# Optimization experiments

Measured on AMD Instinct MI355X. Metric: run time of the kernel, lower is better.

Reference implementation:

```python
import jax, jax.numpy as jnp
import numpy as np

B, S, H, V, NL = 64, 2048, 512, 50257, 2

def setup_inputs() -> dict:
    key = jax.random.key(0)
    ks = jax.random.split(key, 20)
    s = 0.02
    return {
        "input_ids": jax.random.randint(ks[0], (B,), 0, V),
        "hidden": jax.random.normal(ks[1], (NL, B, H), jnp.float32),
        "block_attn_weights": jax.random.uniform(ks[2], (B, 32), jnp.float32),
        "encoder_outputs": jax.random.normal(ks[3], (B, S, H), jnp.float32),
        "n_blocks": 32,
        "emb": jax.random.normal(ks[4], (V, H), jnp.float32) * s,
        "attn_W": jax.random.normal(ks[5], (H, H), jnp.float32) * s,
        "attn_b": jnp.zeros((H,), jnp.float32),
        "W_ih0": jax.random.normal(ks[6], (3 * H, 2 * H), jnp.float32) * s,
        "W_hh0": jax.random.normal(ks[7], (3 * H, H), jnp.float32) * s,
        "b_ih0": jnp.zeros((3 * H,), jnp.float32),
        "b_hh0": jnp.zeros((3 * H,), jnp.float32),
        "W_ih1": jax.random.normal(ks[8], (3 * H, H), jnp.float32) * s,
        "W_hh1": jax.random.normal(ks[9], (3 * H, H), jnp.float32) * s,
        "b_ih1": jnp.zeros((3 * H,), jnp.float32),
        "b_hh1": jnp.zeros((3 * H,), jnp.float32),
        "out_W": jax.random.normal(ks[10], (V, 2 * H), jnp.float32) * s,
        "out_b": jnp.zeros((V,), jnp.float32),
    }

def _gru_cell(x, h, W_ih, W_hh, b_ih, b_hh):
    gx = x @ W_ih.T + b_ih            # [B, 3H]
    gh = h @ W_hh.T + b_hh            # [B, 3H]
    xr, xz, xn = jnp.split(gx, 3, axis=-1)
    hr, hz, hn = jnp.split(gh, 3, axis=-1)
    r = jax.nn.sigmoid(xr + hr)
    z = jax.nn.sigmoid(xz + hz)
    n = jnp.tanh(xn + r * hn)
    return (1.0 - z) * n + z * h

def reference(input_ids, hidden, block_attn_weights, encoder_outputs, n_blocks,
              emb, attn_W, attn_b, W_ih0, W_hh0, b_ih0, b_hh0,
              W_ih1, W_hh1, b_ih1, b_hh1, out_W, out_b):
    b, s, h = encoder_outputs.shape
    L = s // n_blocks
    eo = encoder_outputs.reshape(b, n_blocks, L, h)          # [B,N,L,H]
    # Luong general score: h_dec . (W e + b), per block
    energy = jnp.einsum('bnlh,gh->bnlg', eo, attn_W) + attn_b  # [B,N,L,H]
    scores = jnp.einsum('bh,bnlh->bnl', hidden[-1], energy)    # [B,N,L]
    attn_w = jax.nn.softmax(scores, axis=-1)                   # [B,N,L]
    block_ctx = jnp.einsum('bnl,bnlh->bnh', attn_w, eo)        # [B,N,H]
    context = jnp.einsum('bn,bnh->bh', block_attn_weights, block_ctx)  # [B,H]
    embedded = emb[input_ids]                                  # [B,H]
    x = jnp.concatenate([embedded, context], axis=-1)          # [B,2H]
    h0 = _gru_cell(x, hidden[0], W_ih0, W_hh0, b_ih0, b_hh0)
    h1 = _gru_cell(h0, hidden[1], W_ih1, W_hh1, b_ih1, b_hh1)
    new_hidden = jnp.stack([h0, h1], axis=0)                   # [NL,B,H]
    out_in = jnp.concatenate([h1, context], axis=-1)           # [B,2H]
    log_probs = jax.nn.log_softmax(out_in @ out_W.T + out_b, axis=-1)  # [B,V]
    return (log_probs, new_hidden, context, attn_w)
```

## Files before the change

kernel.cpp:

```cpp
#include <hip/hip_runtime.h>

#define B_  64
#define S_  2048
#define H_  512
#define V_  50257
#define NB_ 32
#define L_  64
#define H3_ 1536
#define NBLK_OUT 786

typedef float  f32x4  __attribute__((ext_vector_type(4)));
typedef __bf16 bf16x8 __attribute__((ext_vector_type(8)));

struct alignas(16) U4 { unsigned int x, y, z, w; };

__device__ __forceinline__ unsigned int f2bf_bits(float f) {
  unsigned int u = __float_as_uint(f);
  return (u + 0x7fffu + ((u >> 16) & 1u)) >> 16;
}

__device__ __forceinline__ f32x4 ntload4(const float* p) {
  return __builtin_nontemporal_load((const f32x4*)p);
}

__device__ __forceinline__ float wave_sum(float v) {
#pragma unroll
  for (int off = 32; off > 0; off >>= 1) v += __shfl_xor(v, off, 64);
  return v;
}

__global__ __launch_bounds__(128) void k_q(const float* __restrict__ hidden,
                                           const float* __restrict__ attn_W,
                                           float* __restrict__ q) {
  __shared__ float sh[4 * H_];
  int tid = threadIdx.x;
  int h  = blockIdx.x * 128 + tid;
  int b0 = blockIdx.y * 4;
  const float* h1 = hidden + B_ * H_;
  for (int i = tid; i < 4 * H_; i += 128) sh[i] = h1[b0 * H_ + i];
  __syncthreads();
  float acc[4] = {0.f, 0.f, 0.f, 0.f};
  for (int g = 0; g < H_; ++g) {
    float w = attn_W[(size_t)g * H_ + h];
#pragma unroll
    for (int bb = 0; bb < 4; ++bb) acc[bb] += sh[bb * H_ + g] * w;
  }
#pragma unroll
  for (int bb = 0; bb < 4; ++bb) q[(b0 + bb) * H_ + h] = acc[bb];
}

__global__ __launch_bounds__(512) void k_attn(
    const float* __restrict__ eo, const float* __restrict__ hidden,
    const float* __restrict__ attn_b, const float* __restrict__ q,
    float* __restrict__ bc, float* __restrict__ attnw_out) {
  __shared__ float sm[8], ss[8];
  __shared__ float shA[8][H_];
  int tid = threadIdx.x;
  int wv = tid >> 6, lane = tid & 63;
  int idx = blockIdx.x;
  int b = idx >> 5, n = idx & 31;

  f32x4 q0 = *(const f32x4*)(q + (size_t)b * H_ + lane * 4);
  f32x4 q1 = *(const f32x4*)(q + (size_t)b * H_ + 256 + lane * 4);

  const float* hp = hidden + (size_t)B_ * H_ + (size_t)b * H_;
  f32x4 hx = *(const f32x4*)(hp + lane * 4);
  f32x4 hy = *(const f32x4*)(hp + 256 + lane * 4);
  f32x4 ax = *(const f32x4*)(attn_b + lane * 4);
  f32x4 ay = *(const f32x4*)(attn_b + 256 + lane * 4);
  float c0 = hx.x*ax.x + hx.y*ax.y + hx.z*ax.z + hx.w*ax.w
           + hy.x*ay.x + hy.y*ay.y + hy.z*ay.z + hy.w*ay.w;
  c0 = wave_sum(c0);

  const float* eb = eo + (size_t)(b * NB_ + n) * L_ * H_;
  float m = -1e30f, s = 0.f, myscore = 0.f;
  f32x4 A0 = {0,0,0,0}, A1 = {0,0,0,0};
  for (int lr = 0; lr < 8; lr += 2) {
    const float* rA = eb + (size_t)(wv * 8 + lr) * H_;
    const float* rB = rA + H_;
    f32x4 a0 = ntload4(rA + lane * 4);
    f32x4 a1 = ntload4(rA + 256 + lane * 4);
    f32x4 b0 = ntload4(rB + lane * 4);
    f32x4 b1 = ntload4(rB + 256 + lane * 4);
    float pa = a0.x*q0.x + a0.y*q0.y + a0.z*q0.z + a0.w*q0.w
             + a1.x*q1.x + a1.y*q1.y + a1.z*q1.z + a1.w*q1.w;
    float pb = b0.x*q0.x + b0.y*q0.y + b0.z*q0.z + b0.w*q0.w
             + b1.x*q1.x + b1.y*q1.y + b1.z*q1.z + b1.w*q1.w;
#pragma unroll
    for (int off = 32; off > 0; off >>= 1) {
      pa += __shfl_xor(pa, off, 64);
      pb += __shfl_xor(pb, off, 64);
    }
    pa += c0; pb += c0;
    if (lane == lr)     myscore = pa;
    if (lane == lr + 1) myscore = pb;
    float mnew  = fmaxf(m, fmaxf(pa, pb));
    float alpha = __expf(m - mnew);
    float wa    = __expf(pa - mnew);
    float wb    = __expf(pb - mnew);
    s = s * alpha + wa + wb;
    A0.x = A0.x*alpha + wa*a0.x + wb*b0.x;
    A0.y = A0.y*alpha + wa*a0.y + wb*b0.y;
    A0.z = A0.z*alpha + wa*a0.z + wb*b0.z;
    A0.w = A0.w*alpha + wa*a0.w + wb*b0.w;
    A1.x = A1.x*alpha + wa*a1.x + wb*b1.x;
    A1.y = A1.y*alpha + wa*a1.y + wb*b1.y;
    A1.z = A1.z*alpha + wa*a1.z + wb*b1.z;
    A1.w = A1.w*alpha + wa*a1.w + wb*b1.w;
    m = mnew;
  }
  if (lane == 0) { sm[wv] = m; ss[wv] = s; }
  __syncthreads();
  float m_g = sm[0];
#pragma unroll
  for (int w = 1; w < 8; ++w) m_g = fmaxf(m_g, sm[w]);
  float s_g = 0.f;
#pragma unroll
  for (int w = 0; w < 8; ++w) s_g += ss[w] * __expf(sm[w] - m_g);
  float scale = __expf(m - m_g);
  f32x4* pa4 = (f32x4*)&shA[wv][0];
  f32x4 w0 = {A0.x*scale, A0.y*scale, A0.z*scale, A0.w*scale};
  f32x4 w1 = {A1.x*scale, A1.y*scale, A1.z*scale, A1.w*scale};
  pa4[lane] = w0; pa4[64 + lane] = w1;
  __syncthreads();
  float inv = 1.f / s_g;
  float sum = 0.f;
#pragma unroll
  for (int w = 0; w < 8; ++w) sum += shA[w][tid];
  bc[(size_t)(b * NB_ + n) * H_ + tid] = sum * inv;
  if (lane < 8)
    attnw_out[(size_t)(b * NB_ + n) * L_ + wv * 8 + lane] =
        __expf(myscore - m_g) * inv;
}

__global__ __launch_bounds__(512) void k_prep(
    const int* __restrict__ ids, const float* __restrict__ hidden,
    const float* __restrict__ baw, const float* __restrict__ emb,
    const float* __restrict__ bc, float* __restrict__ ctx,
    unsigned short* __restrict__ xcatb, unsigned short* __restrict__ h0b,
    unsigned short* __restrict__ h1b, float* __restrict__ out_ctx) {
  int b = blockIdx.x, h = threadIdx.x;
  int id = ids[b];
  float ev = emb[(size_t)id * H_ + h];
  float acc = 0.f;
  for (int n = 0; n < NB_; ++n)
    acc += baw[b * NB_ + n] * bc[(size_t)(b * NB_ + n) * H_ + h];
  ctx[b * H_ + h]      = acc;
  out_ctx[b * H_ + h]  = acc;
  xcatb[b * 1024 + h]        = (unsigned short)f2bf_bits(ev);
  xcatb[b * 1024 + 512 + h]  = (unsigned short)f2bf_bits(acc);
  h0b[b * H_ + h] = (unsigned short)f2bf_bits(hidden[b * H_ + h]);
  h1b[b * H_ + h] = (unsigned short)f2bf_bits(hidden[B_ * H_ + b * H_ + h]);
}

__global__ __launch_bounds__(256) void k_mv2(
    const float* __restrict__ W1, const float* __restrict__ bias1,
    const unsigned short* __restrict__ A1, float* __restrict__ C1, int K1,
    const float* __restrict__ W2, const float* __restrict__ bias2,
    const unsigned short* __restrict__ A2, float* __restrict__ C2, int K2) {
  bool sec = blockIdx.x >= 96;
  const float* W = sec ? W2 : W1;
  const float* bias = sec ? bias2 : bias1;
  const unsigned short* A = sec ? A2 : A1;
  float* C = sec ? C2 : C1;
  int K = sec ? K2 : K1;
  int blk = sec ? blockIdx.x - 96 : blockIdx.x;

  int tid = threadIdx.x;
  int wv = tid >> 6, lane = tid & 63;
  int mrow = lane & 15, qd = lane >> 4;
  int j = blk * 16 + mrow;
  const unsigned short* ap = A + (size_t)(wv * 16 + mrow) * K + qd * 8;
  const float* wp = W + (size_t)j * K + qd * 8;
  f32x4 acc = (f32x4){0.f, 0.f, 0.f, 0.f};
  for (int k0 = 0; k0 < K; k0 += 32) {
    bf16x8 af = __builtin_bit_cast(bf16x8, *(const U4*)(ap + k0));
    f32x4 w0 = *(const f32x4*)(wp + k0);
    f32x4 w1 = *(const f32x4*)(wp + k0 + 4);
    U4 braw;
    braw.x = f2bf_bits(w0.x) | (f2bf_bits(w0.y) << 16);
    braw.y = f2bf_bits(w0.z) | (f2bf_bits(w0.w) << 16);
    braw.z = f2bf_bits(w1.x) | (f2bf_bits(w1.y) << 16);
    braw.w = f2bf_bits(w1.z) | (f2bf_bits(w1.w) << 16);
    bf16x8 bf = __builtin_bit_cast(bf16x8, braw);
    acc = __builtin_amdgcn_mfma_f32_16x16x32_bf16(af, bf, acc, 0, 0, 0);
  }
  float bv = bias[j];
#pragma unroll
  for (int r = 0; r < 4; ++r) {
    int brow = wv * 16 + qd * 4 + r;
    C[(size_t)brow * H3_ + j] = acc[r] + bv;
  }
}

__global__ __launch_bounds__(256) void k_out(
    const float* __restrict__ W, const float* __restrict__ bias,
    const unsigned short* __restrict__ A, float* __restrict__ C,
    float* __restrict__ pm, float* __restrict__ ps) {
  __shared__ float lmS[4][64], lsS[4][64];
  int tid = threadIdx.x;
  int wv = tid >> 6, lane = tid & 63;
  int mrow = lane & 15, qd = lane >> 4;
  int j = blockIdx.x * 64 + wv * 16 + mrow;
  int jc = j < V_ ? j : V_ - 1;
  const float* wp = W + (size_t)jc * 1024 + qd * 8;
  const unsigned short* ap = A + mrow * 1024 + qd * 8;
  f32x4 acc[4];
#pragma unroll
  for (int r = 0; r < 4; ++r) acc[r] = (f32x4){0.f, 0.f, 0.f, 0.f};
  for (int k0 = 0; k0 < 1024; k0 += 32) {
    f32x4 w0 = ntload4(wp + k0);
    f32x4 w1 = ntload4(wp + k0 + 4);
    U4 braw;
    braw.x = f2bf_bits(w0.x) | (f2bf_bits(w0.y) << 16);
    braw.y = f2bf_bits(w0.z) | (f2bf_bits(w0.w) << 16);
    braw.z = f2bf_bits(w1.x) | (f2bf_bits(w1.y) << 16);
    braw.w = f2bf_bits(w1.z) | (f2bf_bits(w1.w) << 16);
    bf16x8 bw = __builtin_bit_cast(bf16x8, braw);
#pragma unroll
    for (int r = 0; r < 4; ++r) {
      bf16x8 af = __builtin_bit_cast(bf16x8, *(const U4*)(ap + r * 16 * 1024 + k0));
      acc[r] = __builtin_amdgcn_mfma_f32_16x16x32_bf16(af, bw, acc[r], 0, 0, 0);
    }
  }
  float bv = (j < V_) ? bias[j] : 0.f;
  if (j < V_) {
#pragma unroll
    for (int r = 0; r < 4; ++r) {
#pragma unroll
      for (int g = 0; g < 4; ++g) {
        int brow = r * 16 + qd * 4 + g;
        C[(size_t)brow * V_ + j] = acc[r][g] + bv;
      }
    }
  }
#pragma unroll
  for (int r = 0; r < 4; ++r) {
#pragma unroll
    for (int g = 0; g < 4; ++g) {
      float v = (j < V_) ? acc[r][g] + bv : -1e30f;
      float mm = v;
#pragma unroll
      for (int off = 1; off <= 8; off <<= 1)
        mm = fmaxf(mm, __shfl_xor(mm, off, 64));
      float se = __expf(v - mm);
#pragma unroll
      for (int off = 1; off <= 8; off <<= 1)
        se += __shfl_xor(se, off, 64);
      if (mrow == 0) {
        int brow = r * 16 + qd * 4 + g;
        lmS[wv][brow] = mm;
        lsS[wv][brow] = se;
      }
    }
  }
  __syncthreads();
  if (tid < 64) {
    float m = lmS[0][tid], s = lsS[0][tid];
#pragma unroll
    for (int w = 1; w < 4; ++w) {
      float mk = lmS[w][tid], sk = lsS[w][tid];
      float mn = fmaxf(m, mk);
      s = s * __expf(m - mn) + sk * __expf(mk - mn);
      m = mn;
    }
    pm[(size_t)tid * NBLK_OUT + blockIdx.x] = m;
    ps[(size_t)tid * NBLK_OUT + blockIdx.x] = s;
  }
}

__global__ __launch_bounds__(512) void k_gru(
    const float* __restrict__ gx, const float* __restrict__ gh,
    const float* __restrict__ hprev, float* __restrict__ hnew_out,
    unsigned short* __restrict__ hnew_bf, const float* __restrict__ ctx,
    unsigned short* __restrict__ outin) {
  int b = blockIdx.x, i = threadIdx.x;
  size_t g0 = (size_t)b * H3_ + i;
  float xr = gx[g0], xz = gx[g0 + 512], xn = gx[g0 + 1024];
  float hr = gh[g0], hz = gh[g0 + 512], hn = gh[g0 + 1024];
  float r  = 1.f / (1.f + __expf(-(xr + hr)));
  float z  = 1.f / (1.f + __expf(-(xz + hz)));
  float nn = tanhf(xn + r * hn);
  float hp = hprev[b * H_ + i];
  float h  = (1.f - z) * nn + z * hp;
  hnew_out[b * H_ + i] = h;
  hnew_bf[b * H_ + i]  = (unsigned short)f2bf_bits(h);
  if (outin) {
    outin[b * 1024 + i]       = (unsigned short)f2bf_bits(h);
    outin[b * 1024 + 512 + i] = (unsigned short)f2bf_bits(ctx[b * H_ + i]);
  }
}

__global__ __launch_bounds__(256) void k_lse(const float* __restrict__ pm,
                                             const float* __restrict__ ps,
                                             float* __restrict__ lse) {
  __shared__ float rm[4], rs[4];
  int b = blockIdx.x, tid = threadIdx.x, lane = tid & 63, wid = tid >> 6;
  float m = -1e30f, s = 0.f;
  for (int k = tid; k < NBLK_OUT; k += 256) {
    float mk = pm[(size_t)b * NBLK_OUT + k];
    float sk = ps[(size_t)b * NBLK_OUT + k];
    float mn = fmaxf(m, mk);
    s = s * __expf(m - mn) + sk * __expf(mk - mn);
    m = mn;
  }
#pragma unroll
  for (int off = 32; off > 0; off >>= 1) {
    float mo = __shfl_xor(m, off, 64);
    float so = __shfl_xor(s, off, 64);
    float mn = fmaxf(m, mo);
    s = s * __expf(m - mn) + so * __expf(mo - mn);
    m = mn;
  }
  if (lane == 0) { rm[wid] = m; rs[wid] = s; }
  __syncthreads();
  if (tid == 0) {
    float mg = rm[0], sg = rs[0];
    for (int w = 1; w < 4; ++w) {
      float mn = fmaxf(mg, rm[w]);
      sg = sg * __expf(mg - mn) + rs[w] * __expf(rm[w] - mn);
      mg = mn;
    }
    lse[b] = mg + logf(sg);
  }
}

__global__ __launch_bounds__(256) void k_wlp(const float* __restrict__ logits,
                                             const float* __restrict__ lse,
                                             float* __restrict__ out) {
  int b = blockIdx.y;
  int j = blockIdx.x * 256 + threadIdx.x;
  if (j < V_) {
    float v = __builtin_nontemporal_load(logits + (size_t)b * V_ + j);
    __builtin_nontemporal_store(v - lse[b], out + (size_t)b * V_ + j);
  }
}

extern "C" void kernel_launch(void* const* d_in, const int* in_sizes, int n_in,
                              void* d_out, int out_size, void* d_ws, size_t ws_size,
                              hipStream_t stream) {
  const int*   ids    = (const int*)d_in[0];
  const float* hidden = (const float*)d_in[1];
  const float* baw    = (const float*)d_in[2];
  const float* eo     = (const float*)d_in[3];
  const float* emb    = (const float*)d_in[5];
  const float* attn_W = (const float*)d_in[6];
  const float* attn_b = (const float*)d_in[7];
  const float* W_ih0  = (const float*)d_in[8];
  const float* W_hh0  = (const float*)d_in[9];
  const float* b_ih0  = (const float*)d_in[10];
  const float* b_hh0  = (const float*)d_in[11];
  const float* W_ih1  = (const float*)d_in[12];
  const float* W_hh1  = (const float*)d_in[13];
  const float* b_ih1  = (const float*)d_in[14];
  const float* b_hh1  = (const float*)d_in[15];
  const float* out_W  = (const float*)d_in[16];
  const float* out_b  = (const float*)d_in[17];
  float* out = (float*)d_out;

  char* ws = (char*)d_ws;
  float*          q      = (float*)(ws + 0);
  float*          bc     = (float*)(ws + 131072);
  float*          ctx    = (float*)(ws + 4325376);
  unsigned short* xcatb  = (unsigned short*)(ws + 4456448);
  unsigned short* h0b    = (unsigned short*)(ws + 4587520);
  unsigned short* h1b    = (unsigned short*)(ws + 4653056);
  unsigned short* h0nb   = (unsigned short*)(ws + 4718592);
  unsigned short* outinb = (unsigned short*)(ws + 4784128);
  float*          gx     = (float*)(ws + 4915200);
  float*          gh     = (float*)(ws + 5308416);
  float*          logits = (float*)(ws + 5701632);
  float*          pm     = (float*)(ws + 18567424);
  float*          ps     = (float*)(ws + 18768640);
  float*          lse    = (float*)(ws + 18969856);

  float* out_lp   = out;
  float* out_nh   = out + 3216448;
  float* out_ctx  = out + 3281984;
  float* out_attw = out + 3314752;

  k_q   <<<dim3(4, 16), 128, 0, stream>>>(hidden, attn_W, q);
  k_attn<<<2048, 512, 0, stream>>>(eo, hidden, attn_b, q, bc, out_attw);
  k_prep<<<64, 512, 0, stream>>>(ids, hidden, baw, emb, bc, ctx, xcatb, h0b, h1b, out_ctx);

  k_mv2<<<192, 256, 0, stream>>>(W_ih0, b_ih0, xcatb, gx, 1024,
                                 W_hh0, b_hh0, h0b,   gh, 512);
  k_gru<<<64, 512, 0, stream>>>(gx, gh, hidden, out_nh, h0nb,
                                (const float*)nullptr, (unsigned short*)nullptr);

  k_mv2<<<192, 256, 0, stream>>>(W_ih1, b_ih1, h0nb, gx, 512,
                                 W_hh1, b_hh1, h1b,  gh, 512);
  k_gru<<<64, 512, 0, stream>>>(gx, gh, hidden + B_ * H_, out_nh + B_ * H_, h0nb,
                                ctx, outinb);

  k_out<<<NBLK_OUT, 256, 0, stream>>>(out_W, out_b, outinb, logits, pm, ps);
  k_lse<<<64, 256, 0, stream>>>(pm, ps, lse);
  k_wlp<<<dim3(197, 64), 256, 0, stream>>>(logits, lse, out_lp);
}
```

Measured before the change: 678.6 us.

## Fuse LSE into log-softmax write, batch attention row loads, use native bf16 cvt

Several unrelated changes land at once. The separate log-sum-exp kernel is folded into the final subtraction kernel, so every block recomputes the row LSE from the partial max/sum arrays and one launch disappears. The attention kernel now loads four encoder rows at a time to get more memory-level parallelism, and writes the attention weights with vector stores from one lane. The manual bf16 rounding is replaced with native __bf16 casts, and the q kernel is split into twice as many blocks. The fused kernel repeats the 786-element reduction in each of its 197 blocks per row, which adds redundant work.

```diff
diff --git a/kernel.cpp b/kernel.cpp
--- a/kernel.cpp
+++ b/kernel.cpp
@@ -23,6 +23,13 @@
   return __builtin_nontemporal_load((const f32x4*)p);
 }
 
+__device__ __forceinline__ bf16x8 cvt8(f32x4 w0, f32x4 w1) {
+  bf16x8 r;
+  r[0] = (__bf16)w0.x; r[1] = (__bf16)w0.y; r[2] = (__bf16)w0.z; r[3] = (__bf16)w0.w;
+  r[4] = (__bf16)w1.x; r[5] = (__bf16)w1.y; r[6] = (__bf16)w1.z; r[7] = (__bf16)w1.w;
+  return r;
+}
+
 __device__ __forceinline__ float wave_sum(float v) {
 #pragma unroll
   for (int off = 32; off > 0; off >>= 1) v += __shfl_xor(v, off, 64);
@@ -32,21 +39,21 @@
 __global__ __launch_bounds__(128) void k_q(const float* __restrict__ hidden,
                                            const float* __restrict__ attn_W,
                                            float* __restrict__ q) {
-  __shared__ float sh[4 * H_];
+  __shared__ float sh[2 * H_];
   int tid = threadIdx.x;
   int h  = blockIdx.x * 128 + tid;
-  int b0 = blockIdx.y * 4;
+  int b0 = blockIdx.y * 2;
   const float* h1 = hidden + B_ * H_;
-  for (int i = tid; i < 4 * H_; i += 128) sh[i] = h1[b0 * H_ + i];
-  __syncthreads();
-  float acc[4] = {0.f, 0.f, 0.f, 0.f};
+  for (int i = tid; i < 2 * H_; i += 128) sh[i] = h1[b0 * H_ + i];
+  __syncthreads();
+  float acc0 = 0.f, acc1 = 0.f;
   for (int g = 0; g < H_; ++g) {
     float w = attn_W[(size_t)g * H_ + h];
-#pragma unroll
-    for (int bb = 0; bb < 4; ++bb) acc[bb] += sh[bb * H_ + g] * w;
-  }
-#pragma unroll
-  for (int bb = 0; bb < 4; ++bb) q[(b0 + bb) * H_ + h] = acc[bb];
+    acc0 += sh[g] * w;
+    acc1 += sh[H_ + g] * w;
+  }
+  q[(b0 + 0) * H_ + h] = acc0;
+  q[(b0 + 1) * H_ + h] = acc1;
 }
 
 __global__ __launch_bounds__(512) void k_attn(
@@ -72,41 +79,44 @@
            + hy.x*ay.x + hy.y*ay.y + hy.z*ay.z + hy.w*ay.w;
   c0 = wave_sum(c0);
 
-  const float* eb = eo + (size_t)(b * NB_ + n) * L_ * H_;
-  float m = -1e30f, s = 0.f, myscore = 0.f;
+  const float* eb = eo + (size_t)(b * NB_ + n) * L_ * H_ + (size_t)(wv * 8) * H_;
+  float m = -1e30f, s = 0.f;
+  float sall[8];
   f32x4 A0 = {0,0,0,0}, A1 = {0,0,0,0};
-  for (int lr = 0; lr < 8; lr += 2) {
-    const float* rA = eb + (size_t)(wv * 8 + lr) * H_;
-    const float* rB = rA + H_;
-    f32x4 a0 = ntload4(rA + lane * 4);
-    f32x4 a1 = ntload4(rA + 256 + lane * 4);
-    f32x4 b0 = ntload4(rB + lane * 4);
-    f32x4 b1 = ntload4(rB + 256 + lane * 4);
-    float pa = a0.x*q0.x + a0.y*q0.y + a0.z*q0.z + a0.w*q0.w
-             + a1.x*q1.x + a1.y*q1.y + a1.z*q1.z + a1.w*q1.w;
-    float pb = b0.x*q0.x + b0.y*q0.y + b0.z*q0.z + b0.w*q0.w
-             + b1.x*q1.x + b1.y*q1.y + b1.z*q1.z + b1.w*q1.w;
+#pragma unroll
+  for (int half = 0; half < 2; ++half) {
+    const float* rb = eb + (size_t)(half * 4) * H_;
+    f32x4 r0[4], r1[4];
+#pragma unroll
+    for (int i = 0; i < 4; ++i) {
+      r0[i] = ntload4(rb + (size_t)i * H_ + lane * 4);
+      r1[i] = ntload4(rb + (size_t)i * H_ + 256 + lane * 4);
+    }
+    float sc[4];
+#pragma unroll
+    for (int i = 0; i < 4; ++i)
+      sc[i] = r0[i].x*q0.x + r0[i].y*q0.y + r0[i].z*q0.z + r0[i].w*q0.w
+            + r1[i].x*q1.x + r1[i].y*q1.y + r1[i].z*q1.z + r1[i].w*q1.w;
 #pragma unroll
     for (int off = 32; off > 0; off >>= 1) {
-      pa += __shfl_xor(pa, off, 64);
-      pb += __shfl_xor(pb, off, 64);
-    }
-    pa += c0; pb += c0;
-    if (lane == lr)     myscore = pa;
-    if (lane == lr + 1) myscore = pb;
-    float mnew  = fmaxf(m, fmaxf(pa, pb));
+#pragma unroll
+      for (int i = 0; i < 4; ++i) sc[i] += __shfl_xor(sc[i], off, 64);
+    }
+    float w[4];
+#pragma unroll
+    for (int i = 0; i < 4; ++i) { sc[i] += c0; sall[half * 4 + i] = sc[i]; }
+    float mloc = fmaxf(fmaxf(sc[0], sc[1]), fmaxf(sc[2], sc[3]));
+    float mnew = fmaxf(m, mloc);
     float alpha = __expf(m - mnew);
-    float wa    = __expf(pa - mnew);
-    float wb    = __expf(pb - mnew);
-    s = s * alpha + wa + wb;
-    A0.x = A0.x*alpha + wa*a0.x + wb*b0.x;
-    A0.y = A0.y*alpha + wa*a0.y + wb*b0.y;
-    A0.z = A0.z*alpha + wa*a0.z + wb*b0.z;
-    A0.w = A0.w*alpha + wa*a0.w + wb*b0.w;
-    A1.x = A1.x*alpha + wa*a1.x + wb*b1.x;
-    A1.y = A1.y*alpha + wa*a1.y + wb*b1.y;
-    A1.z = A1.z*alpha + wa*a1.z + wb*b1.z;
-    A1.w = A1.w*alpha + wa*a1.w + wb*b1.w;
+#pragma unroll
+    for (int i = 0; i < 4; ++i) w[i] = __expf(sc[i] - mnew);
+    s = s * alpha + w[0] + w[1] + w[2] + w[3];
+    A0 *= alpha; A1 *= alpha;
+#pragma unroll
+    for (int i = 0; i < 4; ++i) {
+      A0 += w[i] * r0[i];
+      A1 += w[i] * r1[i];
+    }
     m = mnew;
   }
   if (lane == 0) { sm[wv] = m; ss[wv] = s; }
@@ -119,18 +129,23 @@
   for (int w = 0; w < 8; ++w) s_g += ss[w] * __expf(sm[w] - m_g);
   float scale = __expf(m - m_g);
   f32x4* pa4 = (f32x4*)&shA[wv][0];
-  f32x4 w0 = {A0.x*scale, A0.y*scale, A0.z*scale, A0.w*scale};
-  f32x4 w1 = {A1.x*scale, A1.y*scale, A1.z*scale, A1.w*scale};
-  pa4[lane] = w0; pa4[64 + lane] = w1;
+  pa4[lane]      = A0 * scale;
+  pa4[64 + lane] = A1 * scale;
   __syncthreads();
   float inv = 1.f / s_g;
   float sum = 0.f;
 #pragma unroll
   for (int w = 0; w < 8; ++w) sum += shA[w][tid];
   bc[(size_t)(b * NB_ + n) * H_ + tid] = sum * inv;
-  if (lane < 8)
-    attnw_out[(size_t)(b * NB_ + n) * L_ + wv * 8 + lane] =
-        __expf(myscore - m_g) * inv;
+  if (lane == 0) {
+    f32x4 e0 = {__expf(sall[0]-m_g)*inv, __expf(sall[1]-m_g)*inv,
+                __expf(sall[2]-m_g)*inv, __expf(sall[3]-m_g)*inv};
+    f32x4 e1 = {__expf(sall[4]-m_g)*inv, __expf(sall[5]-m_g)*inv,
+                __expf(sall[6]-m_g)*inv, __expf(sall[7]-m_g)*inv};
+    float* ap_ = attnw_out + (size_t)(b * NB_ + n) * L_ + wv * 8;
+    *(f32x4*)ap_       = e0;
+    *(f32x4*)(ap_ + 4) = e1;
+  }
 }
 
 __global__ __launch_bounds__(512) void k_prep(
@@ -177,12 +192,7 @@
     bf16x8 af = __builtin_bit_cast(bf16x8, *(const U4*)(ap + k0));
     f32x4 w0 = *(const f32x4*)(wp + k0);
     f32x4 w1 = *(const f32x4*)(wp + k0 + 4);
-    U4 braw;
-    braw.x = f2bf_bits(w0.x) | (f2bf_bits(w0.y) << 16);
-    braw.y = f2bf_bits(w0.z) | (f2bf_bits(w0.w) << 16);
-    braw.z = f2bf_bits(w1.x) | (f2bf_bits(w1.y) << 16);
-    braw.w = f2bf_bits(w1.z) | (f2bf_bits(w1.w) << 16);
-    bf16x8 bf = __builtin_bit_cast(bf16x8, braw);
+    bf16x8 bf = cvt8(w0, w1);
     acc = __builtin_amdgcn_mfma_f32_16x16x32_bf16(af, bf, acc, 0, 0, 0);
   }
   float bv = bias[j];
@@ -211,12 +221,7 @@
   for (int k0 = 0; k0 < 1024; k0 += 32) {
     f32x4 w0 = ntload4(wp + k0);
     f32x4 w1 = ntload4(wp + k0 + 4);
-    U4 braw;
-    braw.x = f2bf_bits(w0.x) | (f2bf_bits(w0.y) << 16);
-    braw.y = f2bf_bits(w0.z) | (f2bf_bits(w0.w) << 16);
-    braw.z = f2bf_bits(w1.x) | (f2bf_bits(w1.y) << 16);
-    braw.w = f2bf_bits(w1.z) | (f2bf_bits(w1.w) << 16);
-    bf16x8 bw = __builtin_bit_cast(bf16x8, braw);
+    bf16x8 bw = cvt8(w0, w1);
 #pragma unroll
     for (int r = 0; r < 4; ++r) {
       bf16x8 af = __builtin_bit_cast(bf16x8, *(const U4*)(ap + r * 16 * 1024 + k0));
@@ -291,11 +296,13 @@
   }
 }
 
-__global__ __launch_bounds__(256) void k_lse(const float* __restrict__ pm,
+__global__ __launch_bounds__(256) void k_wlp(const float* __restrict__ logits,
+                                             const float* __restrict__ pm,
                                              const float* __restrict__ ps,
-                                             float* __restrict__ lse) {
+                                             float* __restrict__ out) {
   __shared__ float rm[4], rs[4];
-  int b = blockIdx.x, tid = threadIdx.x, lane = tid & 63, wid = tid >> 6;
+  int tid = threadIdx.x, lane = tid & 63, wid = tid >> 6;
+  int b = blockIdx.y;
   float m = -1e30f, s = 0.f;
   for (int k = tid; k < NBLK_OUT; k += 256) {
     float mk = pm[(size_t)b * NBLK_OUT + k];
@@ -314,25 +321,14 @@
   }
   if (lane == 0) { rm[wid] = m; rs[wid] = s; }
   __syncthreads();
-  if (tid == 0) {
-    float mg = rm[0], sg = rs[0];
-    for (int w = 1; w < 4; ++w) {
-      float mn = fmaxf(mg, rm[w]);
-      sg = sg * __expf(mg - mn) + rs[w] * __expf(rm[w] - mn);
-      mg = mn;
-    }
-    lse[b] = mg + logf(sg);
-  }
-}
-
-__global__ __launch_bounds__(256) void k_wlp(const float* __restrict__ logits,
-                                             const float* __restrict__ lse,
-                                             float* __restrict__ out) {
-  int b = blockIdx.y;
-  int j = blockIdx.x * 256 + threadIdx.x;
+  float mg = fmaxf(fmaxf(rm[0], rm[1]), fmaxf(rm[2], rm[3]));
+  float sg = rs[0] * __expf(rm[0] - mg) + rs[1] * __expf(rm[1] - mg)
+           + rs[2] * __expf(rm[2] - mg) + rs[3] * __expf(rm[3] - mg);
+  float lse = mg + logf(sg);
+  int j = blockIdx.x * 256 + tid;
   if (j < V_) {
     float v = __builtin_nontemporal_load(logits + (size_t)b * V_ + j);
-    __builtin_nontemporal_store(v - lse[b], out + (size_t)b * V_ + j);
+    __builtin_nontemporal_store(v - lse, out + (size_t)b * V_ + j);
   }
 }
 
@@ -372,14 +368,13 @@
   float*          logits = (float*)(ws + 5701632);
   float*          pm     = (float*)(ws + 18567424);
   float*          ps     = (float*)(ws + 18768640);
-  float*          lse    = (float*)(ws + 18969856);
 
   float* out_lp   = out;
   float* out_nh   = out + 3216448;
   float* out_ctx  = out + 3281984;
   float* out_attw = out + 3314752;
 
-  k_q   <<<dim3(4, 16), 128, 0, stream>>>(hidden, attn_W, q);
+  k_q   <<<dim3(4, 32), 128, 0, stream>>>(hidden, attn_W, q);
   k_attn<<<2048, 512, 0, stream>>>(eo, hidden, attn_b, q, bc, out_attw);
   k_prep<<<64, 512, 0, stream>>>(ids, hidden, baw, emb, bc, ctx, xcatb, h0b, h1b, out_ctx);
 
@@ -394,6 +389,5 @@
                                 ctx, outinb);
 
   k_out<<<NBLK_OUT, 256, 0, stream>>>(out_W, out_b, outinb, logits, pm, ps);
-  k_lse<<<64, 256, 0, stream>>>(pm, ps, lse);
-  k_wlp<<<dim3(197, 64), 256, 0, stream>>>(logits, lse, out_lp);
-}
+  k_wlp<<<dim3(197, 64), 256, 0, stream>>>(logits, pm, ps, out_lp);
+}
```

Result: no change. 682.8 us (+0.6%).
